# Kernel optimization log

Hardware: AMD Instinct MI355X
Metric: run time of the kernel (lower is better)

The kernel has to match this reference:

```python
import jax, jax.numpy as jnp
import numpy as np

PATCH = 2  # conv kernel == stride


def _edge_index(h, w):
    """4-neighbor grid edges, plus the module's trailing diagonal edge bug:
    after the loop, (last_node, last_node - w - 1) is appended once."""
    ids = np.arange(h * w, dtype=np.int64).reshape(h, w)
    src = np.concatenate([
        ids[1:, :].ravel(),   # up:    (i, i-w)
        ids[:-1, :].ravel(),  # down:  (i, i+w)
        ids[:, 1:].ravel(),   # left:  (i, i-1)
        ids[:, :-1].ravel(),  # right: (i, i+1)
        np.array([h * w - 1], dtype=np.int64),
    ])
    dst = np.concatenate([
        (ids[1:, :] - w).ravel(),
        (ids[:-1, :] + w).ravel(),
        (ids[:, 1:] - 1).ravel(),
        (ids[:, :-1] + 1).ravel(),
        np.array([h * w - 1 - w - 1], dtype=np.int64),
    ])
    return src, dst


def setup_inputs() -> dict:
    key = jax.random.key(0)
    k1, k2, k3 = jax.random.split(key, 3)
    embed, inc = 192, 3
    x = jax.random.normal(k1, (4, inc, 512, 512), dtype=jnp.float32)
    conv_w = jax.random.normal(k2, (embed, inc, PATCH, PATCH), dtype=jnp.float32) * 0.1
    gcn_w = jax.random.normal(k3, (embed, embed), dtype=jnp.float32) * (1.0 / np.sqrt(embed))
    gcn_b = jnp.zeros((embed,), dtype=jnp.float32)
    return {"x": x, "conv_w": conv_w, "gcn_w": gcn_w, "gcn_b": gcn_b}


def reference(x, conv_w, gcn_w, gcn_b):
    # Patch-embed conv: kernel=stride=PATCH, no bias
    y = jax.lax.conv_general_dilated(
        x, conv_w, window_strides=(PATCH, PATCH), padding='VALID',
        dimension_numbers=('NCHW', 'OIHW', 'NCHW'))
    B, C, H, W = y.shape
    N = H * W
    feats = jnp.transpose(y.reshape(B, C, N), (0, 2, 1)).reshape(B * N, C)  # (B*N, C)

    # GCNConv: linear transform, then symmetric-normalized aggregation with self-loops
    xw = feats @ gcn_w  # (B*N, C)

    src, dst = _edge_index(H, W)  # edges only over first N nodes (faithful to module)
    BN = B * N
    loops = np.arange(BN, dtype=np.int64)  # PyG adds self-loops to ALL B*N nodes
    rows = jnp.asarray(np.concatenate([src, loops]))  # source / message index
    cols = jnp.asarray(np.concatenate([dst, loops]))  # target / aggregate index

    deg = jax.ops.segment_sum(jnp.ones(rows.shape[0], dtype=xw.dtype), cols, num_segments=BN)
    dinv = jnp.where(deg > 0, jax.lax.rsqrt(deg), 0.0)
    norm = dinv[rows] * dinv[cols]  # (E+BN,)

    out = jax.ops.segment_sum(xw[rows] * norm[:, None], cols, num_segments=BN) + gcn_b
    return out.reshape(B, N, C)
```

## Files before the change

### kernel.cpp

```cpp
#include <hip/hip_runtime.h>

#define EMBED 192
#define NPB   64
#define X_HW  512
#define PGRID 256

__global__ __launch_bounds__(192) void wf_kernel(
    const float* __restrict__ conv_w,
    const float* __restrict__ gcn_w,
    float* __restrict__ wf)
{
    const int k  = blockIdx.x;
    const int co = threadIdx.x;
    float s = 0.f;
#pragma unroll 4
    for (int c = 0; c < EMBED; ++c)
        s += conv_w[c * 12 + k] * gcn_w[c * EMBED + co];
    wf[k * EMBED + co] = s;
}

__device__ __forceinline__ float dinv_b0(int ph, int pw) {
    int deg = 1 + (ph > 0) + (ph < PGRID - 1) + (pw > 0) + (pw < PGRID - 1)
                + ((ph == 254) & (pw == 254));
    return rsqrtf((float)deg);
}

__global__ __launch_bounds__(192) void fused_kernel(
    const float* __restrict__ x,
    const float* __restrict__ wf,
    const float* __restrict__ bias,
    float* __restrict__ out)
{
    __shared__ float cp[NPB][13];
    const int tid   = threadIdx.x;
    const int gbase = blockIdx.x * NPB;
    const int b     = gbase >> 16;
    const float* xb0 = x + (size_t)b * 3 * X_HW * X_HW;

#pragma unroll
    for (int it = 0; it < 4; ++it) {
        const int task = it * 192 + tid;
        const int k    = task >> 6;
        const int nl   = task & 63;
        const int n    = (gbase & 65535) + nl;
        const int ph   = n >> 8, pw = n & 255;
        const int ic   = k >> 2, kh = (k >> 1) & 1, kw = k & 1;
        const float* xp = xb0 + (size_t)ic * (X_HW * X_HW)
                        + (ph * 2 + kh) * X_HW + (pw * 2 + kw);
        float v;
        if (b != 0) {
            v = *xp;
        } else {
            const float dn = dinv_b0(ph, pw);
            float acc = dn * dn * (*xp);
            if (ph > 0)         acc += dn * dinv_b0(ph - 1, pw) * xp[-2 * X_HW];
            if (ph < PGRID - 1) acc += dn * dinv_b0(ph + 1, pw) * xp[ 2 * X_HW];
            if (pw > 0)         acc += dn * dinv_b0(ph, pw - 1) * xp[-2];
            if (pw < PGRID - 1) acc += dn * dinv_b0(ph, pw + 1) * xp[ 2];
            if (n == 65278)
                acc += dn * dinv_b0(255, 255) * xp[(255 - ph) * 2 * X_HW + (255 - pw) * 2];
            v = acc;
        }
        cp[nl][k] = v;
    }
    __syncthreads();

    float wfr[12];
#pragma unroll
    for (int k = 0; k < 12; ++k) wfr[k] = wf[k * EMBED + tid];
    const float bco = bias[tid];
    float* op = out + (size_t)gbase * EMBED + tid;
    for (int nl = 0; nl < NPB; ++nl) {
        float acc = bco;
#pragma unroll
        for (int k = 0; k < 12; ++k) acc += cp[nl][k] * wfr[k];
        op[(size_t)nl * EMBED] = acc;
    }
}

extern "C" void kernel_launch(void* const* d_in, const int* in_sizes, int n_in,
                              void* d_out, int out_size, void* d_ws, size_t ws_size,
                              hipStream_t stream) {
    const float* x      = (const float*)d_in[0];
    const float* conv_w = (const float*)d_in[1];
    const float* gcn_w  = (const float*)d_in[2];
    const float* gcn_b  = (const float*)d_in[3];
    float* out = (float*)d_out;
    float* wf  = (float*)d_ws;

    wf_kernel<<<12, EMBED, 0, stream>>>(conv_w, gcn_w, wf);

    const int n_nodes = 4 * PGRID * PGRID;
    fused_kernel<<<n_nodes / NPB, EMBED, 0, stream>>>(x, wf, gcn_b, out);
}
```

Baseline: 237.1 us.

## Replace LDS patch staging with per-wave registers and readlane broadcast

Each wave now loads the 12 patch values for its 64 nodes into registers using float2 loads, and the output loop takes per-node values with readlane instead of going through shared memory. This removes the LDS buffer and the __syncthreads. Each of the three waves in a block loads the same patches redundantly, and the 64-iteration output loop is now fully unrolled. The weight-fold kernel is also repacked into 9 blocks of 256 threads with four independent accumulators.

```diff
diff --git a/kernel.cpp b/kernel.cpp
--- a/kernel.cpp
+++ b/kernel.cpp
@@ -3,26 +3,35 @@
 #define EMBED 192
 #define NPB   64
 #define X_HW  512
-#define PGRID 256
+#define HW2   (X_HW*X_HW)
 
-__global__ __launch_bounds__(192) void wf_kernel(
+__device__ __forceinline__ float dinv_b0(int ph, int pw) {
+    int deg = 1 + (ph > 0) + (ph < 255) + (pw > 0) + (pw < 255)
+                + ((ph == 254) & (pw == 254));
+    return rsqrtf((float)deg);
+}
+
+__device__ __forceinline__ float readlane_f(float v, int lane) {
+    return __int_as_float(__builtin_amdgcn_readlane(__float_as_int(v), lane));
+}
+
+__global__ __launch_bounds__(256) void wf_kernel(
     const float* __restrict__ conv_w,
     const float* __restrict__ gcn_w,
     float* __restrict__ wf)
 {
-    const int k  = blockIdx.x;
-    const int co = threadIdx.x;
-    float s = 0.f;
+    const int idx = blockIdx.x * 256 + threadIdx.x;
+    const int k   = idx / EMBED;
+    const int co  = idx - k * EMBED;
+    float a0 = 0.f, a1 = 0.f, a2 = 0.f, a3 = 0.f;
 #pragma unroll 4
-    for (int c = 0; c < EMBED; ++c)
-        s += conv_w[c * 12 + k] * gcn_w[c * EMBED + co];
-    wf[k * EMBED + co] = s;
-}
-
-__device__ __forceinline__ float dinv_b0(int ph, int pw) {
-    int deg = 1 + (ph > 0) + (ph < PGRID - 1) + (pw > 0) + (pw < PGRID - 1)
-                + ((ph == 254) & (pw == 254));
-    return rsqrtf((float)deg);
+    for (int c = 0; c < EMBED; c += 4) {
+        a0 = fmaf(conv_w[(c+0)*12 + k], gcn_w[(c+0)*EMBED + co], a0);
+        a1 = fmaf(conv_w[(c+1)*12 + k], gcn_w[(c+1)*EMBED + co], a1);
+        a2 = fmaf(conv_w[(c+2)*12 + k], gcn_w[(c+2)*EMBED + co], a2);
+        a3 = fmaf(conv_w[(c+3)*12 + k], gcn_w[(c+3)*EMBED + co], a3);
+    }
+    wf[idx] = (a0 + a1) + (a2 + a3);
 }
 
 __global__ __launch_bounds__(192) void fused_kernel(
@@ -31,49 +40,65 @@
     const float* __restrict__ bias,
     float* __restrict__ out)
 {
-    __shared__ float cp[NPB][13];
     const int tid   = threadIdx.x;
+    const int lane  = tid & 63;
     const int gbase = blockIdx.x * NPB;
     const int b     = gbase >> 16;
-    const float* xb0 = x + (size_t)b * 3 * X_HW * X_HW;
+    const int n     = (gbase & 65535) + lane;
+    const int ph    = n >> 8, pw = n & 255;
+    const float* xp0 = x + (size_t)b * 3 * HW2 + (ph * 2) * X_HW + pw * 2;
 
+    float cp[12];
+    if (b != 0) {
 #pragma unroll
-    for (int it = 0; it < 4; ++it) {
-        const int task = it * 192 + tid;
-        const int k    = task >> 6;
-        const int nl   = task & 63;
-        const int n    = (gbase & 65535) + nl;
-        const int ph   = n >> 8, pw = n & 255;
-        const int ic   = k >> 2, kh = (k >> 1) & 1, kw = k & 1;
-        const float* xp = xb0 + (size_t)ic * (X_HW * X_HW)
-                        + (ph * 2 + kh) * X_HW + (pw * 2 + kw);
-        float v;
-        if (b != 0) {
-            v = *xp;
-        } else {
-            const float dn = dinv_b0(ph, pw);
-            float acc = dn * dn * (*xp);
-            if (ph > 0)         acc += dn * dinv_b0(ph - 1, pw) * xp[-2 * X_HW];
-            if (ph < PGRID - 1) acc += dn * dinv_b0(ph + 1, pw) * xp[ 2 * X_HW];
-            if (pw > 0)         acc += dn * dinv_b0(ph, pw - 1) * xp[-2];
-            if (pw < PGRID - 1) acc += dn * dinv_b0(ph, pw + 1) * xp[ 2];
-            if (n == 65278)
-                acc += dn * dinv_b0(255, 255) * xp[(255 - ph) * 2 * X_HW + (255 - pw) * 2];
-            v = acc;
-        }
-        cp[nl][k] = v;
+        for (int ic = 0; ic < 3; ++ic)
+#pragma unroll
+            for (int kh = 0; kh < 2; ++kh) {
+                const float2 s = *(const float2*)(xp0 + ic * HW2 + kh * X_HW);
+                cp[ic*4 + kh*2 + 0] = s.x;
+                cp[ic*4 + kh*2 + 1] = s.y;
+            }
+    } else {
+        const float dn  = dinv_b0(ph, pw);
+        const float wsf = dn * dn;
+        const float wu  = (ph > 0)   ? dn * dinv_b0(ph-1, pw) : 0.f;
+        const float wd  = (ph < 255) ? dn * dinv_b0(ph+1, pw) : 0.f;
+        const float wl  = (pw > 0)   ? dn * dinv_b0(ph, pw-1) : 0.f;
+        const float wr  = (pw < 255) ? dn * dinv_b0(ph, pw+1) : 0.f;
+        const float wb  = (n == 65278) ? dn * 0.5773502691896258f : 0.f;
+        const int du = (ph > 0)   ? -2 * X_HW : 0;
+        const int dd = (ph < 255) ?  2 * X_HW : 0;
+        const int dl = (pw > 0)   ? -2 : 0;
+        const int dr = (pw < 255) ?  2 : 0;
+        const int db = (255 - ph) * 2 * X_HW + (255 - pw) * 2;
+#pragma unroll
+        for (int ic = 0; ic < 3; ++ic)
+#pragma unroll
+            for (int kh = 0; kh < 2; ++kh) {
+                const float* p = xp0 + ic * HW2 + kh * X_HW;
+                const float2 s  = *(const float2*)(p);
+                const float2 u  = *(const float2*)(p + du);
+                const float2 d  = *(const float2*)(p + dd);
+                const float2 l  = *(const float2*)(p + dl);
+                const float2 r  = *(const float2*)(p + dr);
+                const float2 bg = *(const float2*)(p + db);
+                cp[ic*4+kh*2+0] = wsf*s.x + wu*u.x + wd*d.x + wl*l.x + wr*r.x + wb*bg.x;
+                cp[ic*4+kh*2+1] = wsf*s.y + wu*u.y + wd*d.y + wl*l.y + wr*r.y + wb*bg.y;
+            }
     }
-    __syncthreads();
 
     float wfr[12];
 #pragma unroll
     for (int k = 0; k < 12; ++k) wfr[k] = wf[k * EMBED + tid];
     const float bco = bias[tid];
+
     float* op = out + (size_t)gbase * EMBED + tid;
+#pragma unroll
     for (int nl = 0; nl < NPB; ++nl) {
         float acc = bco;
 #pragma unroll
-        for (int k = 0; k < 12; ++k) acc += cp[nl][k] * wfr[k];
+        for (int k = 0; k < 12; ++k)
+            acc = fmaf(readlane_f(cp[k], nl), wfr[k], acc);
         op[(size_t)nl * EMBED] = acc;
     }
 }
@@ -88,8 +113,8 @@
     float* out = (float*)d_out;
     float* wf  = (float*)d_ws;
 
-    wf_kernel<<<12, EMBED, 0, stream>>>(conv_w, gcn_w, wf);
+    wf_kernel<<<9, 256, 0, stream>>>(conv_w, gcn_w, wf);
 
-    const int n_nodes = 4 * PGRID * PGRID;
-    fused_kernel<<<n_nodes / NPB, EMBED, 0, stream>>>(x, wf, gcn_b, out);
+    const int n_nodes = 4 * 256 * 256;
+    fused_kernel<<<n_nodes / NPB, 192, 0, stream>>>(x, wf, gcn_b, out);
 }
```

Measured after the change: 224.8 us. -5.2%, faster.
